# Performance work log

Measured on AMD Instinct MI355X. Metric: run time of the kernel, lower is better.

Reference implementation:

```python
import jax, jax.numpy as jnp
import numpy as np

V, D, K, NB, T = 50257, 128, 3, 8, 64
DIV_W = 2.0  # diversity_weight


def setup_inputs() -> dict:
    key = jax.random.key(0)
    k1, k2, k3 = jax.random.split(key, 3)
    tokens = jax.random.randint(k1, (T,), 0, V)
    E = jax.random.normal(k2, (V, D), jnp.float32)          # embedding table
    bubbles = 1.5 * jax.random.normal(k3, (K, NB, D), jnp.float32)  # init_spread_foam scale=1.5
    decay_base = jnp.asarray(0.8, jnp.float32)
    sensitivity = jnp.asarray(1.0, jnp.float32)
    return {"tokens": tokens, "E": E, "bubbles": bubbles,
            "decay_base": decay_base, "sensitivity": sensitivity}


def reference(tokens, E, bubbles, decay_base, sensitivity):
    d = E.shape[1]
    inv_sqrt_d = 1.0 / jnp.sqrt(jnp.asarray(d, jnp.float32))
    # normalized bubble states (pure-state directions), fixed over time
    psi = bubbles / (jnp.linalg.norm(bubbles, axis=-1, keepdims=True) + 1e-10)  # [K,NB,D]

    def step(memories, tok):
        # memories: [K, NB, D]
        x = E[tok]  # [D]
        mem_mean = memories.mean(axis=1)  # [K, D]
        mem_norm = jnp.linalg.norm(mem_mean, axis=-1) + 1e-10  # [K]
        x_norm = jnp.linalg.norm(x) + 1e-10
        cos = (mem_mean @ x) / (x_norm * mem_norm)  # [K]
        novelty = jnp.where(mem_norm > 1e-8, 1.0 - cos, 1.0)  # [K]
        decay = jax.nn.sigmoid(decay_base - jnp.abs(sensitivity) * novelty)  # [K]
        xm = x[None, :] + decay[:, None] * mem_mean  # [K, D]

        # foam forward (vectorized over K foams)
        scores = DIV_W * jnp.einsum('knd,kd->kn', bubbles, xm) * inv_sqrt_d  # [K,NB]
        w = jax.nn.softmax(scores, axis=-1)  # [K,NB]
        rho_k = jnp.einsum('kn,knd,kne->kde', w, psi, psi)  # [K,D,D] PSD, trace 1
        eq = w[..., None] * xm[:, None, :] + (1.0 - w)[..., None] * bubbles  # [K,NB,D]
        new_mem = decay[:, None, None] * memories + (1.0 - decay)[:, None, None] * eq

        rho = rho_k.mean(axis=0)  # [D,D] ensemble mixture
        eigs = jnp.clip(jnp.linalg.eigvalsh(rho), 1e-12)
        eigs = eigs / eigs.sum()
        logits = jnp.einsum('vd,de,ve->v', E, rho, E)  # born rule, [V]
        token_probs = jax.nn.softmax(logits)
        S_rho = -(eigs * jnp.clip(jnp.log(eigs), -100.0)).sum()
        H_tokens = -(token_probs * jnp.clip(jnp.log(token_probs), -100.0)).sum()
        F_tokens = H_tokens - S_rho
        logits_k = jnp.einsum('vd,kde,ve->kv', E, rho_k, E)  # [K,V]
        per_foam_probs = jax.nn.softmax(logits_k, axis=-1)
        return new_mem, (token_probs, rho, S_rho, H_tokens, F_tokens, per_foam_probs)

    mem0 = jnp.zeros((bubbles.shape[0], bubbles.shape[1], E.shape[1]), E.dtype)
    _, outs = jax.lax.scan(step, mem0, tokens)
    # outs: token_probs [T,V], rho [T,D,D], S_rho [T], H_tokens [T], F_tokens [T], per_foam_probs [T,K,V]
    return outs
```

## Files before the change

kernel.cpp:

```cpp
#include <hip/hip_runtime.h>
#include <math.h>

namespace {
constexpr int Vv  = 50257;
constexpr int Dc  = 128;
constexpr int Kc  = 3;
constexpr int NBc = 8;
constexpr int Jc  = 24;
constexpr int Tc  = 64;
constexpr int CHV = 1024;
constexpr int NCH = (Vv + CHV - 1) / CHV;
constexpr float INV_SQRT_D = 0.08838834764831845f;
constexpr float DIVW = 2.0f;

constexpr size_t WS_PSI  = 0;
constexpr size_t WS_G    = 4096;
constexpr size_t WS_BB   = 5120;
constexpr size_t WS_XN   = 6144;
constexpr size_t WS_BX   = 6400;
constexpr size_t WS_WALL = 8192;
constexpr size_t WS_PART = 12288;
constexpr size_t WS_LOGZ = 45056;
constexpr size_t WS_P2T  = 65536;

constexpr size_t OFF_TOK = 0;
constexpr size_t OFF_RHO = (size_t)Tc * Vv;
constexpr size_t OFF_S   = OFF_RHO + (size_t)Tc * Dc * Dc;
constexpr size_t OFF_H   = OFF_S + Tc;
constexpr size_t OFF_F   = OFF_H + Tc;
constexpr size_t OFF_PF  = OFF_F + Tc;
}

__device__ __forceinline__ float wsum64(float v) {
#pragma unroll
  for (int m = 1; m < 64; m <<= 1) v += __shfl_xor(v, m);
  return v;
}

__device__ __forceinline__ void comb(float& m1, float& s1, float m2, float s2) {
  float M = fmaxf(m1, m2);
  float e1 = (s1 > 0.f) ? expf(m1 - M) : 0.f;
  float e2 = (s2 > 0.f) ? expf(m2 - M) : 0.f;
  s1 = s1 * e1 + s2 * e2;
  m1 = M;
}
__device__ __forceinline__ void comb_sl(float& m1, float& s1, float& sl1,
                                        float m2, float s2, float sl2) {
  float M = fmaxf(m1, m2);
  float e1 = (s1 > 0.f) ? expf(m1 - M) : 0.f;
  float e2 = (s2 > 0.f) ? expf(m2 - M) : 0.f;
  s1 = s1 * e1 + s2 * e2;
  sl1 = sl1 * e1 + sl2 * e2;
  m1 = M;
}

__global__ void k_prep(const float* __restrict__ bub, float* __restrict__ ws) {
  __shared__ float braw[Jc * Dc];
  __shared__ float psi[Jc * Dc];
  __shared__ float nrm[Jc];
  int tid = threadIdx.x;
  for (int i = tid; i < Jc * Dc; i += 256) braw[i] = bub[i];
  __syncthreads();
  if (tid < Jc) {
    float s = 0.f;
    for (int d = 0; d < Dc; ++d) { float b = braw[tid * Dc + d]; s += b * b; }
    nrm[tid] = sqrtf(s) + 1e-10f;
  }
  __syncthreads();
  for (int i = tid; i < Jc * Dc; i += 256) {
    float v = braw[i] / nrm[i / Dc];
    psi[i] = v;
    ws[WS_PSI + i] = v;
  }
  __syncthreads();
  for (int i = tid; i < Jc * Jc; i += 256) {
    int r = i / Jc, c = i % Jc;
    float g = 0.f, b = 0.f;
    for (int d = 0; d < Dc; ++d) {
      g += psi[r * Dc + d] * psi[c * Dc + d];
      b += braw[r * Dc + d] * braw[c * Dc + d];
    }
    ws[WS_G + i] = g;
    ws[WS_BB + i] = b;
  }
}

__global__ void k_tok(const int* __restrict__ tok, const float* __restrict__ E,
                      const float* __restrict__ bub, float* __restrict__ ws) {
  int t = blockIdx.x, lane = threadIdx.x;
  int tk = tok[t];
  float eA = E[(size_t)tk * Dc + lane];
  float eB = E[(size_t)tk * Dc + 64 + lane];
  float xn = wsum64(eA * eA + eB * eB);
  if (lane == 0) ws[WS_XN + t] = xn;
  float p[Jc];
#pragma unroll
  for (int j = 0; j < Jc; ++j)
    p[j] = bub[j * Dc + lane] * eA + bub[j * Dc + 64 + lane] * eB;
#pragma unroll
  for (int j = 0; j < Jc; ++j) p[j] = wsum64(p[j]);
  if (lane == 0) {
#pragma unroll
    for (int j = 0; j < Jc; ++j) ws[WS_BX + (size_t)t * Jc + j] = p[j];
  }
}

__global__ void k_recur(const int* __restrict__ tok, const float* __restrict__ E,
                        const float* __restrict__ bub, const float* __restrict__ pdb,
                        const float* __restrict__ psn, float* __restrict__ ws) {
  __shared__ float sBX[Tc * Jc];
  __shared__ float sXN[Tc];
  int lane = threadIdx.x;
  for (int i = lane; i < Tc * Jc; i += 64) sBX[i] = ws[WS_BX + i];
  if (lane < Tc) sXN[lane] = ws[WS_XN + lane];
  float db = pdb[0];
  float sens = fabsf(psn[0]);
  int tokv = tok[lane];
  float bubA[Jc], bubB[Jc];
#pragma unroll
  for (int j = 0; j < Jc; ++j) {
    bubA[j] = bub[j * Dc + lane];
    bubB[j] = bub[j * Dc + 64 + lane];
  }
  int jme = (lane < Jc) ? lane : (Jc - 1);
  int kme = jme >> 3;
  float BBrow[Jc];
#pragma unroll
  for (int j = 0; j < Jc; ++j) BBrow[j] = ws[WS_BB + (size_t)jme * Jc + j];
  __syncthreads();
  float mmA[Kc] = {0.f, 0.f, 0.f}, mmB[Kc] = {0.f, 0.f, 0.f};
  float BMv[Kc] = {0.f, 0.f, 0.f};
  int tk0 = __shfl(tokv, 0);
  float xA = E[(size_t)tk0 * Dc + lane];
  float xB = E[(size_t)tk0 * Dc + 64 + lane];
  for (int t = 0; t < Tc; ++t) {
    float nxA = 0.f, nxB = 0.f;
    if (t + 1 < Tc) {
      int nk = __shfl(tokv, t + 1);
      nxA = E[(size_t)nk * Dc + lane];
      nxB = E[(size_t)nk * Dc + 64 + lane];
    }
    float dk[Kc], nk2[Kc];
#pragma unroll
    for (int k = 0; k < Kc; ++k) {
      dk[k]  = wsum64(mmA[k] * xA + mmB[k] * xB);
      nk2[k] = wsum64(mmA[k] * mmA[k] + mmB[k] * mmB[k]);
    }
    float xn = sqrtf(sXN[t]) + 1e-10f;
    float dec[Kc], xmA[Kc], xmB[Kc];
#pragma unroll
    for (int k = 0; k < Kc; ++k) {
      float mn = sqrtf(nk2[k]) + 1e-10f;
      float cosv = dk[k] / (xn * mn);
      float nov = (mn > 1e-8f) ? (1.f - cosv) : 1.f;
      dec[k] = 1.f / (1.f + expf(-(db - sens * nov)));
      xmA[k] = xA + dec[k] * mmA[k];
      xmB[k] = xB + dec[k] * mmB[k];
    }
    float bxj = sBX[t * Jc + jme];
    float decS = (kme == 0) ? dec[0] : ((kme == 1) ? dec[1] : dec[2]);
    float sc = (bxj + decS * BMv[kme]) * (DIVW * INV_SQRT_D);
    float mx = sc;
    mx = fmaxf(mx, __shfl_xor(mx, 1));
    mx = fmaxf(mx, __shfl_xor(mx, 2));
    mx = fmaxf(mx, __shfl_xor(mx, 4));
    float e = expf(sc - mx);
    float ss = e;
    ss += __shfl_xor(ss, 1);
    ss += __shfl_xor(ss, 2);
    ss += __shfl_xor(ss, 4);
    float w = e / ss;
    if (lane < Jc) ws[WS_WALL + (size_t)t * Jc + lane] = w;
    float wj[Jc];
#pragma unroll
    for (int j = 0; j < Jc; ++j) wj[j] = __shfl(w, j);
#pragma unroll
    for (int k = 0; k < Kc; ++k) {
      float accA = 0.f, accB = 0.f;
#pragma unroll
      for (int n = 0; n < NBc; ++n) {
        float om = 1.f - wj[k * NBc + n];
        accA += om * bubA[k * NBc + n];
        accB += om * bubB[k * NBc + n];
      }
      float od8 = (1.f - dec[k]) * 0.125f;
      mmA[k] = dec[k] * mmA[k] + od8 * (xmA[k] + accA);
      mmB[k] = dec[k] * mmB[k] + od8 * (xmB[k] + accB);
    }
#pragma unroll
    for (int k = 0; k < Kc; ++k) {
      float bxm = bxj + dec[k] * BMv[k];
      float s2 = 0.f;
#pragma unroll
      for (int n = 0; n < NBc; ++n) s2 += (1.f - wj[k * NBc + n]) * BBrow[k * NBc + n];
      BMv[k] = dec[k] * BMv[k] + (1.f - dec[k]) * 0.125f * (bxm + s2);
    }
    xA = nxA; xB = nxB;
  }
}

__global__ void k_proj(const float* __restrict__ E, float* __restrict__ ws) {
  __shared__ float4 psi4[Jc][Dc / 4];
  int tid = threadIdx.x;
  for (int i = tid; i < Jc * Dc / 4; i += 256)
    ((float4*)psi4)[i] = ((const float4*)(ws + WS_PSI))[i];
  __syncthreads();
  int v = blockIdx.x * 256 + tid;
  if (v >= Vv) return;
  float acc[Jc];
#pragma unroll
  for (int j = 0; j < Jc; ++j) acc[j] = 0.f;
  const float4* e4 = (const float4*)(E + (size_t)v * Dc);
  for (int d = 0; d < Dc / 4; ++d) {
    float4 e = e4[d];
#pragma unroll
    for (int j = 0; j < Jc; ++j) {
      float4 p = psi4[j][d];
      acc[j] += e.x * p.x + e.y * p.y + e.z * p.z + e.w * p.w;
    }
  }
#pragma unroll
  for (int j = 0; j < Jc; ++j) ws[WS_P2T + (size_t)j * Vv + v] = acc[j] * acc[j];
}

__global__ void k_rho(const float* __restrict__ ws, float* __restrict__ out) {
  int t = blockIdx.x;
  __shared__ float psis[Jc * Dc];
  __shared__ float wsh[Jc];
  int tid = threadIdx.x;
  for (int i = tid; i < Jc * Dc; i += 256) psis[i] = ws[WS_PSI + i];
  if (tid < Jc) wsh[tid] = ws[WS_WALL + (size_t)t * Jc + tid] * (1.f / 3.f);
  __syncthreads();
  int d = tid >> 1, eh = (tid & 1) * 64;
  float4 acc[16];
#pragma unroll
  for (int i = 0; i < 16; ++i) acc[i] = make_float4(0.f, 0.f, 0.f, 0.f);
  for (int j = 0; j < Jc; ++j) {
    float a = wsh[j] * psis[j * Dc + d];
    const float4* pr = (const float4*)&psis[j * Dc + eh];
#pragma unroll
    for (int i = 0; i < 16; ++i) {
      float4 p = pr[i];
      acc[i].x += a * p.x; acc[i].y += a * p.y; acc[i].z += a * p.z; acc[i].w += a * p.w;
    }
  }
  float* o = out + OFF_RHO + (size_t)t * Dc * Dc + (size_t)d * Dc + eh;
#pragma unroll
  for (int i = 0; i < 16; ++i) ((float4*)o)[i] = acc[i];
}

__global__ void k_logits_eig(float* __restrict__ ws, float* __restrict__ out) {
  int ch = blockIdx.x, t = blockIdx.y, tid = threadIdx.x;
  __shared__ float wsh[Jc];
  __shared__ float rm[4][4], rs[4][4], rsl2[4];
  __shared__ float A[Jc * 25];

  if (ch == NCH) {
    if (tid >= 64) return;
    int lane = tid;
    for (int i = lane; i < Jc * Jc; i += 64) {
      int r = i / Jc, c = i % Jc;
      A[r * 25 + c] = ws[WS_G + i] *
                      sqrtf(ws[WS_WALL + (size_t)t * Jc + r] * ws[WS_WALL + (size_t)t * Jc + c]) *
                      (1.f / 3.f);
    }
    __builtin_amdgcn_wave_barrier();
    for (int sweep = 0; sweep < 7; ++sweep) {
      for (int rr = 0; rr < 23; ++rr) {
        float cv = 1.f, sv = 0.f;
        if (lane < Jc) {
          int j = lane;
          int m = (j == 23) ? rr : ((j == rr) ? 23 : (2 * rr + 23 - j) % 23);
          int lo = min(j, m), hi = max(j, m);
          float ajj = A[j * 25 + j];
          float alh = A[lo * 25 + hi];
          float amm = __shfl(ajj, m);
          float app = (j == lo) ? ajj : amm;
          float aqq = (j == lo) ? amm : ajj;
          if (fabsf(alh) > 1e-20f) {
            float th = (aqq - app) / (2.f * alh);
            float tt = 1.f / (fabsf(th) + sqrtf(1.f + th * th));
            if (th < 0.f) tt = -tt;
            cv = 1.f / sqrtf(1.f + tt * tt);
            sv = tt * cv;
          }
        }
        __builtin_amdgcn_wave_barrier();
#pragma unroll
        for (int it = 0; it < 3; ++it) {
          int b = lane + 64 * it;
          int bb = (b < 144) ? b : 143;
          int pi = bb / 12, pj = bb % 12;
          int p0, q0, p1, q1;
          if (pi == 0) { p0 = rr; q0 = 23; }
          else { int a = (rr + pi) % 23, b2 = (rr + 23 - pi) % 23; p0 = min(a, b2); q0 = max(a, b2); }
          if (pj == 0) { p1 = rr; q1 = 23; }
          else { int a = (rr + pj) % 23, b2 = (rr + 23 - pj) % 23; p1 = min(a, b2); q1 = max(a, b2); }
          float ci = __shfl(cv, p0), si = __shfl(sv, p0);
          float cj = __shfl(cv, p1), sj = __shfl(sv, p1);
          if (b < 144) {
            float m00 = A[p0 * 25 + p1], m01 = A[p0 * 25 + q1];
            float m10 = A[q0 * 25 + p1], m11 = A[q0 * 25 + q1];
            float r00 = ci * m00 - si * m10, r01 = ci * m01 - si * m11;
            float r10 = si * m00 + ci * m10, r11 = si * m01 + ci * m11;
            float o00 = cj * r00 - sj * r01, o01 = sj * r00 + cj * r01;
            float o10 = cj * r10 - sj * r11, o11 = sj * r10 + cj * r11;
            A[p0 * 25 + p1] = o00; A[p0 * 25 + q1] = o01;
            A[q0 * 25 + p1] = o10; A[q0 * 25 + q1] = o11;
          }
        }
        __builtin_amdgcn_wave_barrier();
      }
    }
    float lam = 0.f;
    if (lane < Jc) lam = fmaxf(A[lane * 25 + lane], 1e-12f);
    float tot = lam;
#pragma unroll
    for (int off = 32; off; off >>= 1) tot += __shfl_down(tot, off);
    tot = __shfl(tot, 0);
    tot += (float)(Dc - Jc) * 1e-12f;
    float term = 0.f;
    if (lane < Jc) { float p = lam / tot; term = p * logf(p); }
#pragma unroll
    for (int off = 32; off; off >>= 1) term += __shfl_down(term, off);
    if (lane == 0) {
      float pe = 1e-12f / tot;
      out[OFF_S + t] = -(term + (float)(Dc - Jc) * pe * logf(pe));
    }
    return;
  }

  if (tid < Jc) wsh[tid] = ws[WS_WALL + (size_t)t * Jc + tid];
  __syncthreads();
  float m[4] = {-INFINITY, -INFINITY, -INFINITY, -INFINITY};
  float s[4] = {0.f, 0.f, 0.f, 0.f};
  float sl = 0.f;
  const float* p2 = ws + WS_P2T;
  for (int r = 0; r < 4; ++r) {
    int v = ch * CHV + r * 256 + tid;
    if (v >= Vv) break;
    float l0 = 0.f, l1 = 0.f, l2 = 0.f;
#pragma unroll
    for (int n = 0; n < NBc; ++n) {
      l0 += wsh[n]      * p2[(size_t)n * Vv + v];
      l1 += wsh[8 + n]  * p2[(size_t)(8 + n) * Vv + v];
      l2 += wsh[16 + n] * p2[(size_t)(16 + n) * Vv + v];
    }
    float l[4] = { l0, l1, l2, (l0 + l1 + l2) * (1.f / 3.f) };
    out[OFF_TOK + (size_t)t * Vv + v] = l[3];
    out[OFF_PF + ((size_t)t * Kc + 0) * Vv + v] = l0;
    out[OFF_PF + ((size_t)t * Kc + 1) * Vv + v] = l1;
    out[OFF_PF + ((size_t)t * Kc + 2) * Vv + v] = l2;
#pragma unroll
    for (int d = 0; d < 4; ++d) {
      float li = l[d];
      if (li > m[d]) {
        float e = expf(m[d] - li);
        s[d] = s[d] * e + 1.f;
        if (d == 3) sl = sl * e + li;
        m[d] = li;
      } else {
        float e = expf(li - m[d]);
        s[d] += e;
        if (d == 3) sl += e * li;
      }
    }
  }
#pragma unroll
  for (int off = 32; off; off >>= 1) {
#pragma unroll
    for (int d = 0; d < 3; ++d) {
      float om = __shfl_down(m[d], off);
      float os = __shfl_down(s[d], off);
      comb(m[d], s[d], om, os);
    }
    float om = __shfl_down(m[3], off);
    float os = __shfl_down(s[3], off);
    float osl = __shfl_down(sl, off);
    comb_sl(m[3], s[3], sl, om, os, osl);
  }
  int wv = tid >> 6, ln = tid & 63;
  if (ln == 0) {
#pragma unroll
    for (int d = 0; d < 4; ++d) { rm[wv][d] = m[d]; rs[wv][d] = s[d]; }
    rsl2[wv] = sl;
  }
  __syncthreads();
  if (tid == 0) {
    float* part = ws + WS_PART + ((size_t)t * NCH + ch) * 9;
    for (int d = 0; d < 3; ++d) {
      float M = rm[0][d], S = rs[0][d];
      for (int w2 = 1; w2 < 4; ++w2) comb(M, S, rm[w2][d], rs[w2][d]);
      part[d] = M; part[4 + d] = S;
    }
    float M = rm[0][3], S = rs[0][3], SL = rsl2[0];
    for (int w2 = 1; w2 < 4; ++w2) comb_sl(M, S, SL, rm[w2][3], rs[w2][3], rsl2[w2]);
    part[3] = M; part[7] = S; part[8] = SL;
  }
}

__global__ void k_reduce(float* __restrict__ ws, float* __restrict__ out) {
  int t = blockIdx.x, tid = threadIdx.x;
  if (tid < 4) {
    float M = -INFINITY, S = 0.f, SL = 0.f;
    for (int ch = 0; ch < NCH; ++ch) {
      const float* p = ws + WS_PART + ((size_t)t * NCH + ch) * 9;
      if (tid == 3) comb_sl(M, S, SL, p[3], p[7], p[8]);
      else          comb(M, S, p[tid], p[4 + tid]);
    }
    float lz = M + logf(S);
    ws[WS_LOGZ + (size_t)t * 4 + tid] = lz;
    if (tid == 3) {
      float H = lz - SL / S;
      float Srho = out[OFF_S + t];
      out[OFF_H + t] = H;
      out[OFF_F + t] = H - Srho;
    }
  }
}

__global__ void k_norm(const float* __restrict__ ws, float* __restrict__ out, int foam) {
  int row = blockIdx.y, ch = blockIdx.x, tid = threadIdx.x;
  size_t base; int lzi;
  if (foam) { int t = row / Kc, k = row % Kc; base = OFF_PF + (size_t)row * Vv; lzi = t * 4 + k; }
  else { base = OFF_TOK + (size_t)row * Vv; lzi = row * 4 + 3; }
  float lz = ws[WS_LOGZ + lzi];
  for (int r = 0; r < 4; ++r) {
    int v = ch * CHV + r * 256 + tid;
    if (v < Vv) out[base + v] = expf(out[base + v] - lz);
  }
}

extern "C" void kernel_launch(void* const* d_in, const int* in_sizes, int n_in,
                              void* d_out, int out_size, void* d_ws, size_t ws_size,
                              hipStream_t stream) {
  const int*   tokens = (const int*)d_in[0];
  const float* E      = (const float*)d_in[1];
  const float* bub    = (const float*)d_in[2];
  const float* pdb    = (const float*)d_in[3];
  const float* psn    = (const float*)d_in[4];
  float* out = (float*)d_out;
  float* ws  = (float*)d_ws;

  k_prep<<<1, 256, 0, stream>>>(bub, ws);
  k_proj<<<(Vv + 255) / 256, 256, 0, stream>>>(E, ws);
  k_tok<<<Tc, 64, 0, stream>>>(tokens, E, bub, ws);
  k_recur<<<1, 64, 0, stream>>>(tokens, E, bub, pdb, psn, ws);
  k_rho<<<Tc, 256, 0, stream>>>(ws, out);
  k_logits_eig<<<dim3(NCH + 1, Tc), 256, 0, stream>>>(ws, out);
  k_reduce<<<Tc, 64, 0, stream>>>(ws, out);
  k_norm<<<dim3(NCH, Tc), 256, 0, stream>>>(ws, out, 0);
  k_norm<<<dim3(NCH, Tc * Kc), 256, 0, stream>>>(ws, out, 1);
}
```

Measured before the change: 498.4 us.

## Recompute logits in normalize pass instead of storing and rereading outputs

The squared projections are now stored row-major per vocab entry (24 contiguous floats) so each thread reads them with float4 loads. The logits pass no longer writes unnormalized logits to the output. A fused normalize kernel recomputes the logits from the cached projections and writes the final softmax probabilities for all four distributions in one pass. This removes one full write and one read of the large output arrays and merges two normalize launches into one, at the cost of reading the 24-float projection rows twice. Each thread's row reads are strided by 96 bytes across the warp, which is less coalesced than before.

```diff
diff --git a/kernel.cpp b/kernel.cpp
--- a/kernel.cpp
+++ b/kernel.cpp
@@ -52,6 +52,20 @@
   s1 = s1 * e1 + s2 * e2;
   sl1 = sl1 * e1 + sl2 * e2;
   m1 = M;
+}
+
+__device__ __forceinline__ void logits_from_row(const float* __restrict__ p2,
+                                                const float* __restrict__ wsh,
+                                                int v, float& l0, float& l1, float& l2) {
+  const float4* row = (const float4*)(p2 + (size_t)v * Jc);
+  float4 q0 = row[0], q1 = row[1], q2 = row[2], q3 = row[3], q4 = row[4], q5 = row[5];
+  l0 = 0.f; l1 = 0.f; l2 = 0.f;
+  l0 += wsh[0]  * q0.x; l0 += wsh[1]  * q0.y; l0 += wsh[2]  * q0.z; l0 += wsh[3]  * q0.w;
+  l0 += wsh[4]  * q1.x; l0 += wsh[5]  * q1.y; l0 += wsh[6]  * q1.z; l0 += wsh[7]  * q1.w;
+  l1 += wsh[8]  * q2.x; l1 += wsh[9]  * q2.y; l1 += wsh[10] * q2.z; l1 += wsh[11] * q2.w;
+  l1 += wsh[12] * q3.x; l1 += wsh[13] * q3.y; l1 += wsh[14] * q3.z; l1 += wsh[15] * q3.w;
+  l2 += wsh[16] * q4.x; l2 += wsh[17] * q4.y; l2 += wsh[18] * q4.z; l2 += wsh[19] * q4.w;
+  l2 += wsh[20] * q5.x; l2 += wsh[21] * q5.y; l2 += wsh[22] * q5.z; l2 += wsh[23] * q5.w;
 }
 
 __global__ void k_prep(const float* __restrict__ bub, float* __restrict__ ws) {
@@ -219,8 +233,9 @@
       acc[j] += e.x * p.x + e.y * p.y + e.z * p.z + e.w * p.w;
     }
   }
-#pragma unroll
-  for (int j = 0; j < Jc; ++j) ws[WS_P2T + (size_t)j * Vv + v] = acc[j] * acc[j];
+  float* o = ws + WS_P2T + (size_t)v * Jc;
+#pragma unroll
+  for (int j = 0; j < Jc; ++j) o[j] = acc[j] * acc[j];
 }
 
 __global__ void k_rho(const float* __restrict__ ws, float* __restrict__ out) {
@@ -339,18 +354,9 @@
   for (int r = 0; r < 4; ++r) {
     int v = ch * CHV + r * 256 + tid;
     if (v >= Vv) break;
-    float l0 = 0.f, l1 = 0.f, l2 = 0.f;
-#pragma unroll
-    for (int n = 0; n < NBc; ++n) {
-      l0 += wsh[n]      * p2[(size_t)n * Vv + v];
-      l1 += wsh[8 + n]  * p2[(size_t)(8 + n) * Vv + v];
-      l2 += wsh[16 + n] * p2[(size_t)(16 + n) * Vv + v];
-    }
+    float l0, l1, l2;
+    logits_from_row(p2, wsh, v, l0, l1, l2);
     float l[4] = { l0, l1, l2, (l0 + l1 + l2) * (1.f / 3.f) };
-    out[OFF_TOK + (size_t)t * Vv + v] = l[3];
-    out[OFF_PF + ((size_t)t * Kc + 0) * Vv + v] = l0;
-    out[OFF_PF + ((size_t)t * Kc + 1) * Vv + v] = l1;
-    out[OFF_PF + ((size_t)t * Kc + 2) * Vv + v] = l2;
 #pragma unroll
     for (int d = 0; d < 4; ++d) {
       float li = l[d];
@@ -419,15 +425,24 @@
   }
 }
 
-__global__ void k_norm(const float* __restrict__ ws, float* __restrict__ out, int foam) {
-  int row = blockIdx.y, ch = blockIdx.x, tid = threadIdx.x;
-  size_t base; int lzi;
-  if (foam) { int t = row / Kc, k = row % Kc; base = OFF_PF + (size_t)row * Vv; lzi = t * 4 + k; }
-  else { base = OFF_TOK + (size_t)row * Vv; lzi = row * 4 + 3; }
-  float lz = ws[WS_LOGZ + lzi];
+__global__ void k_norm2(const float* __restrict__ ws, float* __restrict__ out) {
+  int ch = blockIdx.x, t = blockIdx.y, tid = threadIdx.x;
+  __shared__ float wsh[Jc];
+  __shared__ float lzs[4];
+  if (tid < Jc) wsh[tid] = ws[WS_WALL + (size_t)t * Jc + tid];
+  if (tid >= 32 && tid < 36) lzs[tid - 32] = ws[WS_LOGZ + (size_t)t * 4 + (tid - 32)];
+  __syncthreads();
+  const float* p2 = ws + WS_P2T;
   for (int r = 0; r < 4; ++r) {
     int v = ch * CHV + r * 256 + tid;
-    if (v < Vv) out[base + v] = expf(out[base + v] - lz);
+    if (v >= Vv) break;
+    float l0, l1, l2;
+    logits_from_row(p2, wsh, v, l0, l1, l2);
+    float l3 = (l0 + l1 + l2) * (1.f / 3.f);
+    out[OFF_TOK + (size_t)t * Vv + v] = expf(l3 - lzs[3]);
+    out[OFF_PF + ((size_t)t * Kc + 0) * Vv + v] = expf(l0 - lzs[0]);
+    out[OFF_PF + ((size_t)t * Kc + 1) * Vv + v] = expf(l1 - lzs[1]);
+    out[OFF_PF + ((size_t)t * Kc + 2) * Vv + v] = expf(l2 - lzs[2]);
   }
 }
 
@@ -449,6 +464,5 @@
   k_rho<<<Tc, 256, 0, stream>>>(ws, out);
   k_logits_eig<<<dim3(NCH + 1, Tc), 256, 0, stream>>>(ws, out);
   k_reduce<<<Tc, 64, 0, stream>>>(ws, out);
-  k_norm<<<dim3(NCH, Tc), 256, 0, stream>>>(ws, out, 0);
-  k_norm<<<dim3(NCH, Tc * Kc), 256, 0, stream>>>(ws, out, 1);
-}
+  k_norm2<<<dim3(NCH, Tc), 256, 0, stream>>>(ws, out);
+}
```

Result: no change. 501.9 us (+0.7%).
